# Kernel optimization log

Measured on AMD Instinct MI355X. Metric: run time of the kernel, lower is better.

## Reference

```python
import jax, jax.numpy as jnp
import numpy as np

N, T, E, B = 50000, 16, 800000, 2000
EMB, ENC, DEC, OUT_LEN = 32, 64, 128, 25
NEG_SLOPE = 0.1
BN_EPS = 1e-5


def lrelu(x):
    return jnp.where(x >= 0, x, NEG_SLOPE * x)


def gru_encode(xs, Wih, Whh, bih, bhh):
    # xs: [T, N, in] -> final hidden [N, H]   (torch GRU gate order: r, z, n)
    H = Whh.shape[1]

    def step(h, x_t):
        gi = x_t @ Wih.T + bih
        gh = h @ Whh.T + bhh
        i_r, i_z, i_n = jnp.split(gi, 3, axis=-1)
        h_r, h_z, h_n = jnp.split(gh, 3, axis=-1)
        r = jax.nn.sigmoid(i_r + h_r)
        z = jax.nn.sigmoid(i_z + h_z)
        n = jnp.tanh(i_n + r * h_n)
        return (1.0 - z) * n + z * h, None

    h0 = jnp.zeros((xs.shape[1], H), xs.dtype)
    hT, _ = jax.lax.scan(step, h0, xs)
    return hT


def lstm_layer(xs, Wih, Whh, bih, bhh):
    # xs: [T, B, in] -> outputs [T, B, H]   (torch LSTM gate order: i, f, g, o)
    H = Whh.shape[1]

    def step(carry, x_t):
        h, c = carry
        g = x_t @ Wih.T + bih + h @ Whh.T + bhh
        i, f, gg, o = jnp.split(g, 4, axis=-1)
        c = jax.nn.sigmoid(f) * c + jax.nn.sigmoid(i) * jnp.tanh(gg)
        h = jax.nn.sigmoid(o) * jnp.tanh(c)
        return (h, c), h

    z0 = jnp.zeros((xs.shape[1], H), xs.dtype)
    _, hs = jax.lax.scan(step, (z0, z0), xs)
    return hs


def cgconv(x, src, dst, edge_attr, Wf, bf, Ws, bs, gamma, beta, mean, var):
    # PyG CGConv: z = [x_i, x_j, e]; msg = sigmoid(lin_f(z)) * softplus(lin_s(z));
    # out = x + BN(scatter_add(msg, i))
    z = jnp.concatenate([x[dst], x[src], edge_attr], axis=-1)  # [E, 2*ENC+2]
    msg = jax.nn.sigmoid(z @ Wf.T + bf) * jax.nn.softplus(z @ Ws.T + bs)
    agg = jax.ops.segment_sum(msg, dst, num_segments=N)  # [N, ENC]
    agg = (agg - mean) * jax.lax.rsqrt(var + BN_EPS) * gamma + beta
    return x + agg


def setup_inputs() -> dict:
    key = jax.random.key(0)
    ks = jax.random.split(key, 32)

    def rn(k, shape, scale=0.1):
        return jax.random.normal(k, shape, jnp.float32) * scale

    inp = {}
    inp["x"] = jax.random.normal(ks[0], (N, T, 2), jnp.float32)
    inp["edge_index"] = jax.random.randint(ks[1], (2, E), 0, N)
    inp["edge_attr"] = jax.random.normal(ks[2], (E, 2), jnp.float32)
    inp["target_index"] = jnp.sort(jax.random.randint(ks[3], (B,), 0, N))
    inp["W_ip"] = rn(ks[4], (EMB, 2)); inp["b_ip"] = jnp.zeros((EMB,), jnp.float32)
    inp["gru_Wih"] = rn(ks[5], (3 * ENC, EMB)); inp["gru_Whh"] = rn(ks[6], (3 * ENC, ENC))
    inp["gru_bih"] = jnp.zeros((3 * ENC,), jnp.float32); inp["gru_bhh"] = jnp.zeros((3 * ENC,), jnp.float32)
    inp["W_dyn"] = rn(ks[7], (ENC, ENC)); inp["b_dyn"] = jnp.zeros((ENC,), jnp.float32)
    Z = 2 * ENC + 2
    for i, base in ((1, 8), (2, 14)):
        inp[f"cg{i}_Wf"] = rn(ks[base], (ENC, Z)); inp[f"cg{i}_bf"] = jnp.zeros((ENC,), jnp.float32)
        inp[f"cg{i}_Ws"] = rn(ks[base + 1], (ENC, Z)); inp[f"cg{i}_bs"] = jnp.zeros((ENC,), jnp.float32)
        inp[f"cg{i}_gamma"] = jnp.ones((ENC,), jnp.float32); inp[f"cg{i}_beta"] = jnp.zeros((ENC,), jnp.float32)
        inp[f"cg{i}_mean"] = jnp.zeros((ENC,), jnp.float32); inp[f"cg{i}_var"] = jnp.ones((ENC,), jnp.float32)
    inp["W_nbrs"] = rn(ks[20], (ENC, ENC)); inp["b_nbrs"] = jnp.zeros((ENC,), jnp.float32)
    inp["lstm0_Wih"] = rn(ks[21], (4 * DEC, 2 * ENC)); inp["lstm0_Whh"] = rn(ks[22], (4 * DEC, DEC))
    inp["lstm0_bih"] = jnp.zeros((4 * DEC,), jnp.float32); inp["lstm0_bhh"] = jnp.zeros((4 * DEC,), jnp.float32)
    inp["lstm1_Wih"] = rn(ks[23], (4 * DEC, DEC)); inp["lstm1_Whh"] = rn(ks[24], (4 * DEC, DEC))
    inp["lstm1_bih"] = jnp.zeros((4 * DEC,), jnp.float32); inp["lstm1_bhh"] = jnp.zeros((4 * DEC,), jnp.float32)
    inp["W_op"] = rn(ks[25], (2, DEC)); inp["b_op"] = jnp.zeros((2,), jnp.float32)
    return inp


def reference(x, edge_index, edge_attr, target_index, W_ip, b_ip,
              gru_Wih, gru_Whh, gru_bih, gru_bhh, W_dyn, b_dyn,
              cg1_Wf, cg1_bf, cg1_Ws, cg1_bs, cg1_gamma, cg1_beta, cg1_mean, cg1_var,
              cg2_Wf, cg2_bf, cg2_Ws, cg2_bs, cg2_gamma, cg2_beta, cg2_mean, cg2_var,
              W_nbrs, b_nbrs,
              lstm0_Wih, lstm0_Whh, lstm0_bih, lstm0_bhh,
              lstm1_Wih, lstm1_Whh, lstm1_bih, lstm1_bhh, W_op, b_op):
    src, dst = edge_index[0], edge_index[1]
    # --- history encoder (GRU) ---
    h = lrelu(x @ W_ip.T + b_ip)                                  # [N, T, EMB]
    hT = gru_encode(h.transpose(1, 0, 2), gru_Wih, gru_Whh, gru_bih, gru_bhh)  # [N, ENC]
    hist = lrelu(lrelu(hT) @ W_dyn.T + b_dyn)                     # [N, ENC]
    # --- CGConv interaction x2 ---
    f = cgconv(hist, src, dst, edge_attr, cg1_Wf, cg1_bf, cg1_Ws, cg1_bs,
               cg1_gamma, cg1_beta, cg1_mean, cg1_var)
    f = cgconv(f, src, dst, edge_attr, cg2_Wf, cg2_bf, cg2_Ws, cg2_bs,
               cg2_gamma, cg2_beta, cg2_mean, cg2_var)
    tar = lrelu(f[target_index] @ W_nbrs.T + b_nbrs)              # [B, ENC]
    enc = jnp.concatenate([hist[target_index], tar], axis=-1)     # [B, 2*ENC]
    # --- LSTM decoder over repeated encoding ---
    xs = jnp.broadcast_to(enc, (OUT_LEN,) + enc.shape)            # [OUT_LEN, B, 2*ENC]
    hs = lstm_layer(xs, lstm0_Wih, lstm0_Whh, lstm0_bih, lstm0_bhh)
    hs = lstm_layer(hs, lstm1_Wih, lstm1_Whh, lstm1_bih, lstm1_bhh)
    fut = hs.transpose(1, 0, 2) @ W_op.T + b_op                   # [B, OUT_LEN, 2]
    return fut
```

## Files before the change

kernel.cpp:

```cpp
#include <hip/hip_runtime.h>
#include <math.h>

#define NN   50000
#define TT   16
#define EE   800000
#define BB   2000
#define EMBD 32
#define ENC  64
#define DEC  128
#define OUTL 25
#define BN_EPS 1e-5f

typedef short v8s __attribute__((ext_vector_type(8)));
typedef float v4f __attribute__((ext_vector_type(4)));
#define MFMA16(a,b,c) __builtin_amdgcn_mfma_f32_16x16x32_bf16((a),(b),(c),0,0,0)

__device__ __forceinline__ float lrelu(float v){ return v >= 0.f ? v : 0.1f*v; }
__device__ __forceinline__ float fsig(float v){ return __builtin_amdgcn_rcpf(1.f + __expf(-v)); }
__device__ __forceinline__ float ftanh(float v){ return 2.f*__builtin_amdgcn_rcpf(1.f + __expf(-2.f*v)) - 1.f; }
__device__ __forceinline__ float fsoftplus(float v){
    return v > 15.f ? v : __logf(1.f + __expf(v));
}
__device__ __forceinline__ float hsum(float4 a){ return (a.x+a.y)+(a.z+a.w); }

__device__ __forceinline__ unsigned short f2bf(float f){
    unsigned u = __float_as_uint(f);
    u = u + 0x7FFFu + ((u>>16)&1u);
    return (unsigned short)(u>>16);
}
__device__ __forceinline__ float bf2f(unsigned short s){ return __uint_as_float(((unsigned)s)<<16); }

__device__ __forceinline__ v8s as_v8s(int4 v){
    union { int4 i; v8s s; } u; u.i = v; return u.s;
}

__device__ __forceinline__ void cvt8(const float* p, v8s& hi, v8s& lo){
    float4 a0 = *(const float4*)p;
    float4 a1 = *(const float4*)(p+4);
    float av[8] = {a0.x,a0.y,a0.z,a0.w,a1.x,a1.y,a1.z,a1.w};
#pragma unroll
    for (int j=0;j<8;j++){
        unsigned short h = f2bf(av[j]);
        hi[j] = (short)h;
        lo[j] = (short)f2bf(av[j] - bf2f(h));
    }
}
__device__ __forceinline__ void lrelu_resplit(v8s hh, v8s hl, v8s& oh, v8s& ol){
#pragma unroll
    for (int j=0;j<8;j++){
        float v = bf2f((unsigned short)hh[j]) + bf2f((unsigned short)hl[j]);
        float a = lrelu(v);
        unsigned short h = f2bf(a);
        oh[j] = (short)h;
        ol[j] = (short)f2bf(a - bf2f(h));
    }
}

__device__ __forceinline__ void pf_item(const float* W, int K, int KB, int i,
                                        unsigned short* out){
    int l = i & 63, fb = i >> 6;
    int kb = fb % KB, nt = fb / KB;
    int n = nt*16 + (l&15);
    int k0 = kb*32 + ((l>>4)*8);
#pragma unroll
    for (int j=0;j<8;j++) out[i*8+j] = f2bf(W[(size_t)n*K + k0 + j]);
}
__device__ __forceinline__ void phl_item(const float* W, int K, int KB, int i,
                                         unsigned short* hi, unsigned short* lo){
    int l = i & 63, fb = i >> 6;
    int kb = fb % KB, nt = fb / KB;
    int n = nt*16 + (l&15);
    int k0 = kb*32 + ((l>>4)*8);
#pragma unroll
    for (int j=0;j<8;j++){
        float v = W[(size_t)n*K + k0 + j];
        unsigned short h = f2bf(v);
        hi[i*8+j] = h;
        lo[i*8+j] = f2bf(v - bf2f(h));
    }
}
__device__ __forceinline__ void pcat_item(const float* Wa, const float* Wb,
                                          int K1, int K, int KB, int i,
                                          unsigned short* out){
    int l = i & 63, fb = i >> 6;
    int kb = fb % KB, nt = fb / KB;
    int n = nt*16 + (l&15);
    int k0 = kb*32 + ((l>>4)*8);
#pragma unroll
    for (int j=0;j<8;j++){
        int k = k0 + j;
        float v = (k < K1) ? Wa[(size_t)n*K1 + k] : Wb[(size_t)n*(K-K1) + (k-K1)];
        out[i*8+j] = f2bf(v);
    }
}
__device__ __forceinline__ void pproj_item(const float* Wf, const float* Ws, int i,
                                           unsigned short* hi, unsigned short* lo){
    int l = i & 63, fb = i >> 6;
    int kb = fb & 1, nt = fb >> 1;
    int n = nt*16 + (l&15);
    int d = n >> 6, c = n & 63;
    const float* W = (d < 2) ? Wf : Ws;
    int k0 = (d&1)*64 + kb*32 + ((l>>4)*8);
#pragma unroll
    for (int j=0;j<8;j++){
        float v = W[c*130 + k0 + j];
        unsigned short h = f2bf(v);
        hi[i*8+j] = h;
        lo[i*8+j] = f2bf(v - bf2f(h));
    }
}

__global__ void pack_all(
    const float* __restrict__ gWih, const float* __restrict__ gWhh,
    const float* __restrict__ Wdyn,
    const float* __restrict__ l0Whh, const float* __restrict__ l1Wih,
    const float* __restrict__ l1Whh, const float* __restrict__ l0Wih,
    const float* __restrict__ c1Wf, const float* __restrict__ c1Ws,
    const float* __restrict__ c2Wf, const float* __restrict__ c2Ws,
    unsigned short* __restrict__ pWih, unsigned short* __restrict__ pWhh,
    unsigned short* __restrict__ pWdyn,
    unsigned short* __restrict__ B0h, unsigned short* __restrict__ B1h,
    unsigned short* __restrict__ P1h, unsigned short* __restrict__ P1l,
    unsigned short* __restrict__ P2h, unsigned short* __restrict__ P2l,
    unsigned short* __restrict__ GIh, unsigned short* __restrict__ GIl,
    int* __restrict__ cnt, int* __restrict__ gtot)
{
    int i = blockIdx.x*256 + threadIdx.x;
    if (i < 768){ pf_item(gWih, 32, 1, i, pWih); return; }   i -= 768;
    if (i < 1536){ pf_item(gWhh, 64, 2, i, pWhh); return; }  i -= 1536;
    if (i < 512){ pf_item(Wdyn, 64, 2, i, pWdyn); return; }  i -= 512;
    if (i < 8192){ pcat_item(l0Whh, l0Whh, 128, 128, 4, i, B0h); return; } i -= 8192;
    if (i < 16384){ pcat_item(l1Wih, l1Whh, 128, 256, 8, i, B1h); return; } i -= 16384;
    if (i < 2048){ pproj_item(c1Wf, c1Ws, i, P1h, P1l); return; } i -= 2048;
    if (i < 2048){ pproj_item(c2Wf, c2Ws, i, P2h, P2l); return; } i -= 2048;
    if (i < 8192){ phl_item(l0Wih, 128, 4, i, GIh, GIl); return; } i -= 8192;
    if (i < NN){ cnt[i] = 0; return; } i -= NN;
    if (i < 1){ gtot[0] = 0; return; }
}
#define PACK_TOTAL (768+1536+512+8192+16384+2048+2048+8192+NN+1)

__global__ __launch_bounds__(128) void encoder_mfma(
    const float* __restrict__ x,
    const float* __restrict__ Wip, const float* __restrict__ bip,
    const unsigned short* __restrict__ pWih,
    const unsigned short* __restrict__ pWhh,
    const float* __restrict__ bih, const float* __restrict__ bhh,
    const unsigned short* __restrict__ pWdyn,
    const float* __restrict__ bdyn,
    float* __restrict__ hist)
{
    __shared__ float sxl[512];
    __shared__ unsigned short efh[512], efl[512];
    __shared__ unsigned short hfh[2*512], hfl[2*512];
    const int tid = threadIdx.x;
    const int l   = tid & 63;
    const int w   = tid >> 6;
    const int ln  = l & 15, q = l >> 4;
    const int blk = blockIdx.x;

    ((float4*)sxl)[tid] = ((const float4*)x)[(size_t)blk*128 + tid];
    for (int i=tid;i<2*512;i+=128){ hfh[i]=0; hfl[i]=0; }

    const int ek = tid & 31;
    const float w0 = Wip[2*ek], w1 = Wip[2*ek+1], bk = bip[ek];
    const int em0 = tid >> 5;
    const int eoffb = (16*(ek>>3))*8 + (ek&7);

    float bR[2], bZ[2], bNI[2], bNH[2];
    float hprev[2][4];
#pragma unroll
    for (int u=0;u<2;u++){
        int g = 2*w + u;
        int c = g*16 + ln;
        bR[u]  = bih[c]       + bhh[c];
        bZ[u]  = bih[64 + c]  + bhh[64 + c];
        bNI[u] = bih[128 + c];
        bNH[u] = bhh[128 + c];
        hprev[u][0]=0.f; hprev[u][1]=0.f; hprev[u][2]=0.f; hprev[u][3]=0.f;
    }
    const v8s* FIH = (const v8s*)pWih;
    const v8s* FHH = (const v8s*)pWhh;
    const v8s* FDY = (const v8s*)pWdyn;
    __syncthreads();

#pragma unroll 1
    for (int t=0;t<TT;t++){
#pragma unroll
        for (int r=0;r<4;r++){
            int m = em0 + r*4;
            float e = lrelu(w0*sxl[m*32 + 2*t] + w1*sxl[m*32 + 2*t + 1] + bk);
            unsigned short h_ = f2bf(e);
            int off = eoffb + m*8;
            efh[off] = h_;
            efl[off] = f2bf(e - bf2f(h_));
        }
        __syncthreads();
        v8s eh = *(const v8s*)&efh[l*8];
        v8s el = *(const v8s*)&efl[l*8];
        v8s h0h = *(const v8s*)&hfh[l*8];
        v8s h0l = *(const v8s*)&hfl[l*8];
        v8s h1h = *(const v8s*)&hfh[512 + l*8];
        v8s h1l = *(const v8s*)&hfl[512 + l*8];
        __syncthreads();
#pragma unroll
        for (int u=0;u<2;u++){
            int g = 2*w + u;
            v4f aR = {bR[u],bR[u],bR[u],bR[u]};
            v4f aZ = {bZ[u],bZ[u],bZ[u],bZ[u]};
            v4f aNI= {bNI[u],bNI[u],bNI[u],bNI[u]};
            v4f aNH= {bNH[u],bNH[u],bNH[u],bNH[u]};
            v8s b;
            b = FIH[(g   )*64 + l];   aR = MFMA16(eh,b,aR);  aR = MFMA16(el,b,aR);
            b = FHH[((g)*2+0)*64+l];  aR = MFMA16(h0h,b,aR); aR = MFMA16(h0l,b,aR);
            b = FHH[((g)*2+1)*64+l];  aR = MFMA16(h1h,b,aR); aR = MFMA16(h1l,b,aR);
            b = FIH[(4+g )*64 + l];   aZ = MFMA16(eh,b,aZ);  aZ = MFMA16(el,b,aZ);
            b = FHH[((4+g)*2+0)*64+l];aZ = MFMA16(h0h,b,aZ); aZ = MFMA16(h0l,b,aZ);
            b = FHH[((4+g)*2+1)*64+l];aZ = MFMA16(h1h,b,aZ); aZ = MFMA16(h1l,b,aZ);
            b = FIH[(8+g )*64 + l];   aNI= MFMA16(eh,b,aNI); aNI= MFMA16(el,b,aNI);
            b = FHH[((8+g)*2+0)*64+l];aNH= MFMA16(h0h,b,aNH);aNH= MFMA16(h0l,b,aNH);
            b = FHH[((8+g)*2+1)*64+l];aNH= MFMA16(h1h,b,aNH);aNH= MFMA16(h1l,b,aNH);
#pragma unroll
            for (int i=0;i<4;i++){
                float r_ = fsig(aR[i]);
                float z_ = fsig(aZ[i]);
                float nn_ = ftanh(aNI[i] + r_*aNH[i]);
                float hn = (1.f - z_)*nn_ + z_*hprev[u][i];
                hprev[u][i] = hn;
                int row = q*4 + i, col = g*16 + ln;
                int off = (col>>5)*512 + (16*((col&31)>>3) + row)*8 + (col&7);
                unsigned short hh_ = f2bf(hn);
                hfh[off] = hh_;
                hfl[off] = f2bf(hn - bf2f(hh_));
            }
        }
    }
    __syncthreads();
    {
        v8s a0h,a0l,a1h,a1l;
        lrelu_resplit(*(const v8s*)&hfh[l*8],       *(const v8s*)&hfl[l*8],       a0h, a0l);
        lrelu_resplit(*(const v8s*)&hfh[512 + l*8], *(const v8s*)&hfl[512 + l*8], a1h, a1l);
#pragma unroll
        for (int u=0;u<2;u++){
            int nt = 2*w + u;
            float bb = bdyn[nt*16 + ln];
            v4f acc = {bb,bb,bb,bb};
            v8s b;
            b = FDY[(nt*2+0)*64 + l]; acc = MFMA16(a0h,b,acc); acc = MFMA16(a0l,b,acc);
            b = FDY[(nt*2+1)*64 + l]; acc = MFMA16(a1h,b,acc); acc = MFMA16(a1l,b,acc);
#pragma unroll
            for (int i=0;i<4;i++){
                hist[(size_t)(blk*16 + q*4 + i)*64 + nt*16 + ln] = lrelu(acc[i]);
            }
        }
    }
}

__global__ __launch_bounds__(256) void proj_mfma(
    const float* __restrict__ xin,
    const unsigned short* __restrict__ Bh, const unsigned short* __restrict__ Bl,
    float* __restrict__ Af, float* __restrict__ Bf,
    float* __restrict__ As, float* __restrict__ Bs)
{
    __shared__ float sx[64*68];
    const int tid = threadIdx.x;
    const int l = tid & 63;
    const int w = tid >> 6;
    const int ln = l & 15, q = l >> 4;
    const int n0 = blockIdx.x*64;

    for (int i=tid;i<64*16;i+=256){
        int nn = i>>4, f4 = i&15;
        float4 v = {0.f,0.f,0.f,0.f};
        if (n0+nn < NN) v = ((const float4*)(xin + (size_t)(n0+nn)*64))[f4];
        *(float4*)&sx[nn*68 + f4*4] = v;
    }
    __syncthreads();

    v8s ah0,al0,ah1,al1;
    cvt8(&sx[(w*16+ln)*68 +      q*8], ah0, al0);
    cvt8(&sx[(w*16+ln)*68 + 32 + q*8], ah1, al1);

    const v8s* FH = (const v8s*)Bh;
    const v8s* FL = (const v8s*)Bl;
#pragma unroll 1
    for (int nt=0; nt<16; nt++){
        v8s bh0 = FH[(nt*2+0)*64 + l], bl0 = FL[(nt*2+0)*64 + l];
        v8s bh1 = FH[(nt*2+1)*64 + l], bl1 = FL[(nt*2+1)*64 + l];
        v4f acc = {0.f,0.f,0.f,0.f};
        acc = MFMA16(ah0,bh0,acc); acc = MFMA16(al0,bh0,acc); acc = MFMA16(ah0,bl0,acc);
        acc = MFMA16(ah1,bh1,acc); acc = MFMA16(al1,bh1,acc); acc = MFMA16(ah1,bl1,acc);
        int d = nt >> 2, col = (nt&3)*16 + ln;
        float* op = (d==0) ? Af : (d==1) ? Bf : (d==2) ? As : Bs;
#pragma unroll
        for (int i=0;i<4;i++){
            int node = n0 + w*16 + q*4 + i;
            if (node < NN) op[(size_t)node*64 + col] = acc[i];
        }
    }
}

__global__ void count_kernel(const int* __restrict__ ei, int* __restrict__ cnt){
    int e = blockIdx.x*256 + threadIdx.x;
    if (e < EE) atomicAdd(&cnt[ei[EE+e]], 1);
}

__global__ void alloc_kernel(const int* __restrict__ cnt, int* __restrict__ gtot,
                             int* __restrict__ off, int* __restrict__ cur){
    int n = blockIdx.x*256 + threadIdx.x;
    if (n >= NN) return;
    int c = cnt[n];
    int s = atomicAdd(gtot, c);
    off[n] = s;
    cur[n] = s;
}

__global__ void scatter_kernel(const int* __restrict__ ei, const float* __restrict__ ea,
                               int* __restrict__ cur, int4* __restrict__ recS){
    int e = blockIdx.x*256 + threadIdx.x;
    if (e >= EE) return;
    int d = ei[EE+e];
    int p = atomicAdd(&cur[d], 1);
    int4 r;
    r.x = ei[e];
    r.y = __float_as_int(ea[2*(size_t)e]);
    r.z = __float_as_int(ea[2*(size_t)e+1]);
    r.w = 0;
    recS[p] = r;
}

__global__ __launch_bounds__(256) void cg_agg(
    const float* __restrict__ xin,
    const int4* __restrict__ recS,
    const int* __restrict__ off, const int* __restrict__ cnt,
    const float* __restrict__ Wf, const float* __restrict__ bf,
    const float* __restrict__ Ws, const float* __restrict__ bs,
    const float* __restrict__ Af, const float* __restrict__ Bf,
    const float* __restrict__ As, const float* __restrict__ Bs,
    const float* __restrict__ gamma, const float* __restrict__ beta,
    const float* __restrict__ mean, const float* __restrict__ var,
    float* __restrict__ outp)
{
    const int tid = threadIdx.x;
    const int c = tid & 63, wid = tid >> 6;
    const int n = blockIdx.x*4 + wid;
    if (n >= NN) return;

    const float wf0 = Wf[c*130+128], wf1 = Wf[c*130+129], bfc = bf[c];
    const float ws0 = Ws[c*130+128], ws1 = Ws[c*130+129], bsc = bs[c];
    const float afd = Af[(size_t)n*64+c] + bfc, asd = As[(size_t)n*64+c] + bsc;
    const float* Bfc = Bf + c;
    const float* Bsc = Bs + c;

    float acc = 0.f;
    int i = off[n];
    const int i1 = i + cnt[n];
#pragma unroll 1
    for (; i+1 < i1; i += 2){
        int4 r0 = recS[i], r1 = recS[i+1];
        float e00 = __int_as_float(r0.y), e01 = __int_as_float(r0.z);
        float e10 = __int_as_float(r1.y), e11 = __int_as_float(r1.z);
        float bf0v = Bfc[(size_t)r0.x*64], bs0v = Bsc[(size_t)r0.x*64];
        float bf1v = Bfc[(size_t)r1.x*64], bs1v = Bsc[(size_t)r1.x*64];
        float gf0 = afd + bf0v + wf0*e00 + wf1*e01;
        float gs0 = asd + bs0v + ws0*e00 + ws1*e01;
        float gf1 = afd + bf1v + wf0*e10 + wf1*e11;
        float gs1 = asd + bs1v + ws0*e10 + ws1*e11;
        acc += fsig(gf0)*fsoftplus(gs0);
        acc += fsig(gf1)*fsoftplus(gs1);
    }
    if (i < i1){
        int4 r0 = recS[i];
        float e00 = __int_as_float(r0.y), e01 = __int_as_float(r0.z);
        float gf = afd + Bfc[(size_t)r0.x*64] + wf0*e00 + wf1*e01;
        float gs = asd + Bsc[(size_t)r0.x*64] + ws0*e00 + ws1*e01;
        acc += fsig(gf)*fsoftplus(gs);
    }
    float bn = (acc - mean[c])*rsqrtf(var[c]+BN_EPS)*gamma[c] + beta[c];
    outp[(size_t)n*64+c] = xin[(size_t)n*64+c] + bn;
}

__global__ __launch_bounds__(256) void target_kernel(
    const float* __restrict__ hist, const float* __restrict__ f2,
    const int* __restrict__ tgt,
    const float* __restrict__ Wn, const float* __restrict__ bn_,
    float* __restrict__ enc)
{
    const int tid=threadIdx.x;
    const int c = tid&63, q = tid>>6;
    const int b = blockIdx.x*4 + q;
    if (b>=BB) return;
    const int n = tgt[b];
    float a = bn_[c];
#pragma unroll
    for (int k=0;k<ENC;k++) a += Wn[c*64+k]*f2[(size_t)n*64+k];
    enc[(size_t)b*128 + 64 + c] = lrelu(a);
    enc[(size_t)b*128 + c]      = hist[(size_t)n*64+c];
}

__global__ __launch_bounds__(512) void gi0_mfma(
    const float* __restrict__ enc,
    const unsigned short* __restrict__ GIh, const unsigned short* __restrict__ GIl,
    const float* __restrict__ bih0, const float* __restrict__ bhh0,
    float* __restrict__ gi0)
{
    __shared__ float senc[16*132];
    const int tid = threadIdx.x;
    const int l = tid & 63;
    const int w = tid >> 6;
    const int ln = l & 15, q = l >> 4;
    const int b0 = blockIdx.x*16;

    for (int i=tid;i<16*32;i+=512){
        int row = i>>5, f4 = i&31;
        *(float4*)&senc[row*132 + f4*4] = ((const float4*)(enc + (size_t)(b0+row)*128))[f4];
    }
    __syncthreads();

    v8s ah[4], al[4];
#pragma unroll
    for (int kb=0;kb<4;kb++) cvt8(&senc[ln*132 + kb*32 + q*8], ah[kb], al[kb]);

    const v8s* FH = (const v8s*)GIh;
    const v8s* FL = (const v8s*)GIl;
#pragma unroll
    for (int u=0;u<4;u++){
        int nt = w*4 + u;
        int col = nt*16 + ln;
        float bb = bih0[col] + bhh0[col];
        v4f acc = {bb,bb,bb,bb};
#pragma unroll
        for (int kb=0;kb<4;kb++){
            v8s bh = FH[(nt*4+kb)*64 + l];
            v8s bl = FL[(nt*4+kb)*64 + l];
            acc = MFMA16(ah[kb],bh,acc); acc = MFMA16(al[kb],bh,acc); acc = MFMA16(ah[kb],bl,acc);
        }
#pragma unroll
        for (int i=0;i<4;i++)
            gi0[(size_t)(b0 + q*4 + i)*512 + col] = acc[i];
    }
}

#define LMB 16
__global__ __launch_bounds__(512)
__attribute__((amdgpu_waves_per_eu(2,2)))
void lstm_mfma(
    const float* __restrict__ gi0,
    const unsigned short* __restrict__ B0h,
    const unsigned short* __restrict__ B1h,
    const float* __restrict__ bih1, const float* __restrict__ bhh1,
    const float* __restrict__ Wop, const float* __restrict__ bop,
    float* __restrict__ outp)
{
    __shared__ int4 sW0[32*4*64];
    __shared__ unsigned short h0hi[2][4*512], h0lo[2][4*512];
    __shared__ unsigned short h1hi[2][4*512], h1lo[2][4*512];
    const int tid = threadIdx.x;
    const int l = tid & 63;
    const int w = tid >> 6;
    const int c = l & 15;
    const int q = l >> 4;
    const int j = w*16 + c;
    const int b0 = blockIdx.x*LMB;

    {
        const int4* F0 = (const int4*)B0h;
        for (int i=tid;i<32*4*64;i+=512) sW0[i] = F0[i];
    }
    for (int i=tid;i<4*512;i+=512){
        h0hi[0][i]=0; h0lo[0][i]=0; h0hi[1][i]=0; h0lo[1][i]=0;
        h1hi[0][i]=0; h1lo[0][i]=0; h1hi[1][i]=0; h1lo[1][i]=0;
    }

    int4 W1r[32];
    {
        const int4* F1 = (const int4*)B1h;
#pragma unroll
        for (int g=0;g<4;g++)
#pragma unroll
            for (int kb=0;kb<8;kb++) W1r[g*8+kb] = F1[((g*8+w)*8 + kb)*64 + l];
#pragma unroll
        for (int i=0;i<32;i++)
            asm volatile("" : "+v"(W1r[i].x), "+v"(W1r[i].y), "+v"(W1r[i].z), "+v"(W1r[i].w));
    }

    float rgi[4][4];
#pragma unroll
    for (int g=0;g<4;g++)
#pragma unroll
        for (int i=0;i<4;i++)
            rgi[g][i] = gi0[(size_t)(b0 + q*4 + i)*512 + g*128 + j];

    float b1[4];
#pragma unroll
    for (int g=0;g<4;g++) b1[g] = bih1[g*128+j] + bhh1[g*128+j];
    float c0[4] = {0,0,0,0}, c1[4] = {0,0,0,0};
    const float wop0 = Wop[j], wop1 = Wop[128 + j];
    const float bo0 = bop[0], bo1 = bop[1];
    const int kbw = j>>5, qw = (j>>3)&3, jw = j&7;
    __syncthreads();

    int p = 0;
#pragma unroll 1
    for (int t=0;t<OUTL;t++){
        v4f aH[4], aL[4];
#pragma unroll
        for (int g=0;g<4;g++){
            v4f t4 = {rgi[g][0], rgi[g][1], rgi[g][2], rgi[g][3]};
            aH[g] = t4;
            v4f z = {0.f,0.f,0.f,0.f};
            aL[g] = z;
        }
#pragma unroll
        for (int kb=0;kb<4;kb++){
            v8s ah = *(const v8s*)&h0hi[p][kb*512 + l*8];
            v8s al = *(const v8s*)&h0lo[p][kb*512 + l*8];
#pragma unroll
            for (int g=0;g<4;g++){
                v8s bfr = as_v8s(sW0[((g*8+w)*4 + kb)*64 + l]);
                aH[g] = MFMA16(ah, bfr, aH[g]);
                aL[g] = MFMA16(al, bfr, aL[g]);
            }
        }
#pragma unroll
        for (int i=0;i<4;i++){
            float gi_ = aH[0][i]+aL[0][i], gf_ = aH[1][i]+aL[1][i];
            float gg_ = aH[2][i]+aL[2][i], go_ = aH[3][i]+aL[3][i];
            c0[i] = fsig(gf_)*c0[i] + fsig(gi_)*ftanh(gg_);
            float hn = fsig(go_)*ftanh(c0[i]);
            int off = kbw*512 + (qw*16 + q*4 + i)*8 + jw;
            unsigned short h = f2bf(hn);
            h0hi[1-p][off] = h;
            h0lo[1-p][off] = f2bf(hn - bf2f(h));
        }
        __syncthreads();

        v4f bH[4], bL[4];
#pragma unroll
        for (int g=0;g<4;g++){
            v4f t4={b1[g],b1[g],b1[g],b1[g]}; bH[g]=t4;
            v4f z={0.f,0.f,0.f,0.f}; bL[g]=z;
        }
#pragma unroll
        for (int kb=0;kb<8;kb++){
            const unsigned short* hb = (kb<4) ? h0hi[1-p] : h1hi[p];
            const unsigned short* lb = (kb<4) ? h0lo[1-p] : h1lo[p];
            int kk = kb & 3;
            v8s ah = *(const v8s*)&hb[kk*512 + l*8];
            v8s al = *(const v8s*)&lb[kk*512 + l*8];
#pragma unroll
            for (int g=0;g<4;g++){
                bH[g] = MFMA16(ah, as_v8s(W1r[g*8+kb]), bH[g]);
                bL[g] = MFMA16(al, as_v8s(W1r[g*8+kb]), bL[g]);
            }
        }
        float h1new[4];
#pragma unroll
        for (int i=0;i<4;i++){
            float gi_ = bH[0][i]+bL[0][i], gf_ = bH[1][i]+bL[1][i];
            float gg_ = bH[2][i]+bL[2][i], go_ = bH[3][i]+bL[3][i];
            c1[i] = fsig(gf_)*c1[i] + fsig(gi_)*ftanh(gg_);
            h1new[i] = fsig(go_)*ftanh(c1[i]);
            int off = kbw*512 + (qw*16 + q*4 + i)*8 + jw;
            unsigned short h = f2bf(h1new[i]);
            h1hi[1-p][off] = h;
            h1lo[1-p][off] = f2bf(h1new[i] - bf2f(h));
        }

        {
            float v0[4], v1[4];
#pragma unroll
            for (int i=0;i<4;i++){ v0[i] = h1new[i]*wop0; v1[i] = h1new[i]*wop1; }
#pragma unroll
            for (int m=1;m<16;m<<=1){
#pragma unroll
                for (int i=0;i<4;i++){
                    v0[i] += __shfl_xor(v0[i], m);
                    v1[i] += __shfl_xor(v1[i], m);
                }
            }
            if (c == 0){
                if (w == 0){
#pragma unroll
                    for (int i=0;i<4;i++){ v0[i] += bo0; v1[i] += bo1; }
                }
#pragma unroll
                for (int i=0;i<4;i++){
                    size_t base = (size_t)(b0 + q*4 + i)*(OUTL*2) + t*2;
                    atomicAdd(&outp[base    ], v0[i]);
                    atomicAdd(&outp[base + 1], v1[i]);
                }
            }
        }
        p ^= 1;
    }
}

extern "C" void kernel_launch(void* const* d_in, const int* in_sizes, int n_in,
                              void* d_out, int out_size, void* d_ws, size_t ws_size,
                              hipStream_t stream)
{
    const float* x    = (const float*)d_in[0];
    const int*   ei   = (const int*)d_in[1];
    const float* ea   = (const float*)d_in[2];
    const int*   tgt  = (const int*)d_in[3];
    const float* Wip  = (const float*)d_in[4];
    const float* bip  = (const float*)d_in[5];
    const float* gWih = (const float*)d_in[6];
    const float* gWhh = (const float*)d_in[7];
    const float* gbih = (const float*)d_in[8];
    const float* gbhh = (const float*)d_in[9];
    const float* Wdyn = (const float*)d_in[10];
    const float* bdyn = (const float*)d_in[11];
    const float* c1Wf=(const float*)d_in[12]; const float* c1bf=(const float*)d_in[13];
    const float* c1Ws=(const float*)d_in[14]; const float* c1bs=(const float*)d_in[15];
    const float* c1g =(const float*)d_in[16]; const float* c1b =(const float*)d_in[17];
    const float* c1m =(const float*)d_in[18]; const float* c1v =(const float*)d_in[19];
    const float* c2Wf=(const float*)d_in[20]; const float* c2bf=(const float*)d_in[21];
    const float* c2Ws=(const float*)d_in[22]; const float* c2bs=(const float*)d_in[23];
    const float* c2g =(const float*)d_in[24]; const float* c2b =(const float*)d_in[25];
    const float* c2m =(const float*)d_in[26]; const float* c2v =(const float*)d_in[27];
    const float* Wn  =(const float*)d_in[28]; const float* bn_ =(const float*)d_in[29];
    const float* l0Wih=(const float*)d_in[30]; const float* l0Whh=(const float*)d_in[31];
    const float* l0bih=(const float*)d_in[32]; const float* l0bhh=(const float*)d_in[33];
    const float* l1Wih=(const float*)d_in[34]; const float* l1Whh=(const float*)d_in[35];
    const float* l1bih=(const float*)d_in[36]; const float* l1bhh=(const float*)d_in[37];
    const float* Wop =(const float*)d_in[38]; const float* bop=(const float*)d_in[39];

    float* ws = (float*)d_ws;
    size_t o = 0;
    float* hist = ws + o; o += (size_t)NN*ENC;
    float* f1   = ws + o; o += (size_t)NN*ENC;
    float* f2   = ws + o; o += (size_t)NN*ENC;
    float* Af   = ws + o; o += (size_t)NN*ENC;
    float* Bf   = ws + o; o += (size_t)NN*ENC;
    float* As   = ws + o; o += (size_t)NN*ENC;
    float* Bs   = ws + o; o += (size_t)NN*ENC;
    float* enc  = ws + o; o += (size_t)BB*2*ENC;
    float* gi0  = ws + o; o += (size_t)BB*4*DEC;
    unsigned short* pWih  = (unsigned short*)(ws + o); o += (size_t)12*64*8/2;
    unsigned short* pWhh  = (unsigned short*)(ws + o); o += (size_t)24*64*8/2;
    unsigned short* pWdyn = (unsigned short*)(ws + o); o += (size_t)8*64*8/2;
    unsigned short* B0h = (unsigned short*)(ws + o); o += (size_t)32*4*64*8/2;
    unsigned short* B1h = (unsigned short*)(ws + o); o += (size_t)32*8*64*8/2;
    unsigned short* P1h = (unsigned short*)(ws + o); o += (size_t)2048*8/2;
    unsigned short* P1l = (unsigned short*)(ws + o); o += (size_t)2048*8/2;
    unsigned short* P2h = (unsigned short*)(ws + o); o += (size_t)2048*8/2;
    unsigned short* P2l = (unsigned short*)(ws + o); o += (size_t)2048*8/2;
    unsigned short* GIh = (unsigned short*)(ws + o); o += (size_t)8192*8/2;
    unsigned short* GIl = (unsigned short*)(ws + o); o += (size_t)8192*8/2;
    int* cnt    = (int*)(ws + o); o += NN;
    int* offv   = (int*)(ws + o); o += NN+1;
    int* curv   = (int*)(ws + o); o += NN;
    int* gtot   = (int*)(ws + o); o += 1;
    o = (o + 3) & ~(size_t)3;
    int4* recS  = (int4*)(ws + o); o += (size_t)4*EE;

    pack_all<<<(PACK_TOTAL+255)/256, 256, 0, stream>>>(
        gWih, gWhh, Wdyn, l0Whh, l1Wih, l1Whh, l0Wih,
        c1Wf, c1Ws, c2Wf, c2Ws,
        pWih, pWhh, pWdyn, B0h, B1h, P1h, P1l, P2h, P2l, GIh, GIl, cnt, gtot);

    (void)hipMemsetAsync(d_out, 0, (size_t)out_size*sizeof(float), stream);

    count_kernel<<<(EE+255)/256, 256, 0, stream>>>(ei, cnt);
    alloc_kernel<<<(NN+255)/256, 256, 0, stream>>>(cnt, gtot, offv, curv);
    scatter_kernel<<<(EE+255)/256, 256, 0, stream>>>(ei, ea, curv, recS);

    encoder_mfma<<<NN/16, 128, 0, stream>>>(x, Wip, bip, pWih, pWhh, gbih, gbhh, pWdyn, bdyn, hist);

    proj_mfma<<<(NN+63)/64, 256, 0, stream>>>(hist, P1h, P1l, Af,Bf,As,Bs);
    cg_agg<<<(NN+3)/4, 256, 0, stream>>>(hist, recS, offv, cnt,
                                         c1Wf,c1bf,c1Ws,c1bs, Af,Bf,As,Bs,
                                         c1g,c1b,c1m,c1v, f1);

    proj_mfma<<<(NN+63)/64, 256, 0, stream>>>(f1, P2h, P2l, Af,Bf,As,Bs);
    cg_agg<<<(NN+3)/4, 256, 0, stream>>>(f1, recS, offv, cnt,
                                         c2Wf,c2bf,c2Ws,c2bs, Af,Bf,As,Bs,
                                         c2g,c2b,c2m,c2v, f2);

    target_kernel<<<(BB+3)/4, 256, 0, stream>>>(hist, f2, tgt, Wn, bn_, enc);

    gi0_mfma<<<BB/16, 512, 0, stream>>>(enc, GIh, GIl, l0bih, l0bhh, gi0);

    lstm_mfma<<<BB/LMB, 512, 0, stream>>>(gi0, B0h, B1h,
                                          l1bih, l1bhh, Wop, bop, (float*)d_out);
}
```

Measured before the change: 627.7 us.

## Run GRU encoder with one wavefront per block and register-built embeddings

The GRU encoder block shrinks from two wavefronts to one, and that wave now handles all four 16-column gate groups. The input embedding is computed straight into MFMA A-operand registers from a transposed LDS copy of x, which removes the embedding LDS staging and one barrier per timestep. The fp32-to-bf16 hi/lo split switches from round-to-nearest to a cheaper truncation. In exchange, the grid has half as many waves and each wave runs a longer serial MFMA chain per step, and the split's rounding behaviour changes slightly.

```diff
diff --git a/kernel.cpp b/kernel.cpp
--- a/kernel.cpp
+++ b/kernel.cpp
@@ -29,6 +29,13 @@
     return (unsigned short)(u>>16);
 }
 __device__ __forceinline__ float bf2f(unsigned short s){ return __uint_as_float(((unsigned)s)<<16); }
+
+__device__ __forceinline__ void tsplit(float v, unsigned short& hi, unsigned short& lo){
+    unsigned u = __float_as_uint(v);
+    hi = (unsigned short)(u >> 16);
+    float r = v - __uint_as_float(u & 0xFFFF0000u);
+    lo = (unsigned short)(__float_as_uint(r) >> 16);
+}
 
 __device__ __forceinline__ v8s as_v8s(int4 v){
     union { int4 i; v8s s; } u; u.i = v; return u.s;
@@ -139,7 +146,7 @@
 }
 #define PACK_TOTAL (768+1536+512+8192+16384+2048+2048+8192+NN+1)
 
-__global__ __launch_bounds__(128) void encoder_mfma(
+__global__ __launch_bounds__(64) void encoder_mfma(
     const float* __restrict__ x,
     const float* __restrict__ Wip, const float* __restrict__ bip,
     const unsigned short* __restrict__ pWih,
@@ -149,34 +156,36 @@
     const float* __restrict__ bdyn,
     float* __restrict__ hist)
 {
-    __shared__ float sxl[512];
-    __shared__ unsigned short efh[512], efl[512];
-    __shared__ unsigned short hfh[2*512], hfl[2*512];
+    __shared__ float sxt[512];
+    __shared__ unsigned short hfh[1024], hfl[1024];
     const int tid = threadIdx.x;
-    const int l   = tid & 63;
-    const int w   = tid >> 6;
+    const int l   = tid;
     const int ln  = l & 15, q = l >> 4;
     const int blk = blockIdx.x;
 
-    ((float4*)sxl)[tid] = ((const float4*)x)[(size_t)blk*128 + tid];
-    for (int i=tid;i<2*512;i+=128){ hfh[i]=0; hfl[i]=0; }
-
-    const int ek = tid & 31;
-    const float w0 = Wip[2*ek], w1 = Wip[2*ek+1], bk = bip[ek];
-    const int em0 = tid >> 5;
-    const int eoffb = (16*(ek>>3))*8 + (ek&7);
-
-    float bR[2], bZ[2], bNI[2], bNH[2];
-    float hprev[2][4];
-#pragma unroll
-    for (int u=0;u<2;u++){
-        int g = 2*w + u;
+    for (int idx = tid; idx < 512; idx += 64){
+        int m = idx >> 5, r = idx & 31;
+        sxt[(r>>1)*32 + m*2 + (r&1)] = x[(size_t)blk*512 + idx];
+    }
+    for (int i = tid; i < 1024; i += 64){ hfh[i] = 0; hfl[i] = 0; }
+
+    float w0[8], w1[8], bk[8];
+#pragma unroll
+    for (int j = 0; j < 8; j++){
+        int k = q*8 + j;
+        w0[j] = Wip[2*k]; w1[j] = Wip[2*k+1]; bk[j] = bip[k];
+    }
+
+    float bR[4], bZ[4], bNI[4], bNH[4];
+    float hprev[4][4];
+#pragma unroll
+    for (int g = 0; g < 4; g++){
         int c = g*16 + ln;
-        bR[u]  = bih[c]       + bhh[c];
-        bZ[u]  = bih[64 + c]  + bhh[64 + c];
-        bNI[u] = bih[128 + c];
-        bNH[u] = bhh[128 + c];
-        hprev[u][0]=0.f; hprev[u][1]=0.f; hprev[u][2]=0.f; hprev[u][3]=0.f;
+        bR[g]  = bih[c]       + bhh[c];
+        bZ[g]  = bih[64 + c]  + bhh[64 + c];
+        bNI[g] = bih[128 + c];
+        bNH[g] = bhh[128 + c];
+        hprev[g][0]=0.f; hprev[g][1]=0.f; hprev[g][2]=0.f; hprev[g][3]=0.f;
     }
     const v8s* FIH = (const v8s*)pWih;
     const v8s* FHH = (const v8s*)pWhh;
@@ -184,71 +193,66 @@
     __syncthreads();
 
 #pragma unroll 1
-    for (int t=0;t<TT;t++){
-#pragma unroll
-        for (int r=0;r<4;r++){
-            int m = em0 + r*4;
-            float e = lrelu(w0*sxl[m*32 + 2*t] + w1*sxl[m*32 + 2*t + 1] + bk);
-            unsigned short h_ = f2bf(e);
-            int off = eoffb + m*8;
-            efh[off] = h_;
-            efl[off] = f2bf(e - bf2f(h_));
-        }
-        __syncthreads();
-        v8s eh = *(const v8s*)&efh[l*8];
-        v8s el = *(const v8s*)&efl[l*8];
+    for (int t = 0; t < TT; t++){
+        float2 xv = *(const float2*)&sxt[t*32 + ln*2];
+        v8s eh, el;
+#pragma unroll
+        for (int j = 0; j < 8; j++){
+            float e = lrelu(w0[j]*xv.x + w1[j]*xv.y + bk[j]);
+            unsigned short h_, l_;
+            tsplit(e, h_, l_);
+            eh[j] = (short)h_; el[j] = (short)l_;
+        }
         v8s h0h = *(const v8s*)&hfh[l*8];
         v8s h0l = *(const v8s*)&hfl[l*8];
         v8s h1h = *(const v8s*)&hfh[512 + l*8];
         v8s h1l = *(const v8s*)&hfl[512 + l*8];
-        __syncthreads();
-#pragma unroll
-        for (int u=0;u<2;u++){
-            int g = 2*w + u;
-            v4f aR = {bR[u],bR[u],bR[u],bR[u]};
-            v4f aZ = {bZ[u],bZ[u],bZ[u],bZ[u]};
-            v4f aNI= {bNI[u],bNI[u],bNI[u],bNI[u]};
-            v4f aNH= {bNH[u],bNH[u],bNH[u],bNH[u]};
+#pragma unroll
+        for (int g = 0; g < 4; g++){
+            v4f aR = {bR[g],bR[g],bR[g],bR[g]};
+            v4f aZ = {bZ[g],bZ[g],bZ[g],bZ[g]};
+            v4f aNI= {bNI[g],bNI[g],bNI[g],bNI[g]};
+            v4f aNH= {bNH[g],bNH[g],bNH[g],bNH[g]};
             v8s b;
-            b = FIH[(g   )*64 + l];   aR = MFMA16(eh,b,aR);  aR = MFMA16(el,b,aR);
-            b = FHH[((g)*2+0)*64+l];  aR = MFMA16(h0h,b,aR); aR = MFMA16(h0l,b,aR);
-            b = FHH[((g)*2+1)*64+l];  aR = MFMA16(h1h,b,aR); aR = MFMA16(h1l,b,aR);
-            b = FIH[(4+g )*64 + l];   aZ = MFMA16(eh,b,aZ);  aZ = MFMA16(el,b,aZ);
-            b = FHH[((4+g)*2+0)*64+l];aZ = MFMA16(h0h,b,aZ); aZ = MFMA16(h0l,b,aZ);
-            b = FHH[((4+g)*2+1)*64+l];aZ = MFMA16(h1h,b,aZ); aZ = MFMA16(h1l,b,aZ);
-            b = FIH[(8+g )*64 + l];   aNI= MFMA16(eh,b,aNI); aNI= MFMA16(el,b,aNI);
-            b = FHH[((8+g)*2+0)*64+l];aNH= MFMA16(h0h,b,aNH);aNH= MFMA16(h0l,b,aNH);
-            b = FHH[((8+g)*2+1)*64+l];aNH= MFMA16(h1h,b,aNH);aNH= MFMA16(h1l,b,aNH);
-#pragma unroll
-            for (int i=0;i<4;i++){
+            b = FIH[(g   )*64 + l];    aR = MFMA16(eh,b,aR);  aR = MFMA16(el,b,aR);
+            b = FHH[(g*2+0)*64+l];     aR = MFMA16(h0h,b,aR); aR = MFMA16(h0l,b,aR);
+            b = FHH[(g*2+1)*64+l];     aR = MFMA16(h1h,b,aR); aR = MFMA16(h1l,b,aR);
+            b = FIH[(4+g )*64 + l];    aZ = MFMA16(eh,b,aZ);  aZ = MFMA16(el,b,aZ);
+            b = FHH[((4+g)*2+0)*64+l]; aZ = MFMA16(h0h,b,aZ); aZ = MFMA16(h0l,b,aZ);
+            b = FHH[((4+g)*2+1)*64+l]; aZ = MFMA16(h1h,b,aZ); aZ = MFMA16(h1l,b,aZ);
+            b = FIH[(8+g )*64 + l];    aNI= MFMA16(eh,b,aNI); aNI= MFMA16(el,b,aNI);
+            b = FHH[((8+g)*2+0)*64+l]; aNH= MFMA16(h0h,b,aNH);aNH= MFMA16(h0l,b,aNH);
+            b = FHH[((8+g)*2+1)*64+l]; aNH= MFMA16(h1h,b,aNH);aNH= MFMA16(h1l,b,aNH);
+#pragma unroll
+            for (int i = 0; i < 4; i++){
                 float r_ = fsig(aR[i]);
                 float z_ = fsig(aZ[i]);
                 float nn_ = ftanh(aNI[i] + r_*aNH[i]);
-                float hn = (1.f - z_)*nn_ + z_*hprev[u][i];
-                hprev[u][i] = hn;
+                float hn = (1.f - z_)*nn_ + z_*hprev[g][i];
+                hprev[g][i] = hn;
                 int row = q*4 + i, col = g*16 + ln;
                 int off = (col>>5)*512 + (16*((col&31)>>3) + row)*8 + (col&7);
-                unsigned short hh_ = f2bf(hn);
+                unsigned short hh_, hl_;
+                tsplit(hn, hh_, hl_);
                 hfh[off] = hh_;
-                hfl[off] = f2bf(hn - bf2f(hh_));
+                hfl[off] = hl_;
             }
         }
-    }
-    __syncthreads();
+        __syncthreads();
+    }
     {
         v8s a0h,a0l,a1h,a1l;
         lrelu_resplit(*(const v8s*)&hfh[l*8],       *(const v8s*)&hfl[l*8],       a0h, a0l);
         lrelu_resplit(*(const v8s*)&hfh[512 + l*8], *(const v8s*)&hfl[512 + l*8], a1h, a1l);
 #pragma unroll
-        for (int u=0;u<2;u++){
-            int nt = 2*w + u;
+        for (int nt = 0; nt < 4; nt++){
             float bb = bdyn[nt*16 + ln];
             v4f acc = {bb,bb,bb,bb};
             v8s b;
             b = FDY[(nt*2+0)*64 + l]; acc = MFMA16(a0h,b,acc); acc = MFMA16(a0l,b,acc);
             b = FDY[(nt*2+1)*64 + l]; acc = MFMA16(a1h,b,acc); acc = MFMA16(a1l,b,acc);
 #pragma unroll
-            for (int i=0;i<4;i++){
+            for (int i = 0; i < 4; i++){
                 hist[(size_t)(blk*16 + q*4 + i)*64 + nt*16 + ln] = lrelu(acc[i]);
             }
         }
@@ -666,7 +670,7 @@
     alloc_kernel<<<(NN+255)/256, 256, 0, stream>>>(cnt, gtot, offv, curv);
     scatter_kernel<<<(EE+255)/256, 256, 0, stream>>>(ei, ea, curv, recS);
 
-    encoder_mfma<<<NN/16, 128, 0, stream>>>(x, Wip, bip, pWih, pWhh, gbih, gbhh, pWdyn, bdyn, hist);
+    encoder_mfma<<<NN/16, 64, 0, stream>>>(x, Wip, bip, pWih, pWhh, gbih, gbhh, pWdyn, bdyn, hist);
 
     proj_mfma<<<(NN+63)/64, 256, 0, stream>>>(hist, P1h, P1l, Af,Bf,As,Bs);
     cg_agg<<<(NN+3)/4, 256, 0, stream>>>(hist, recS, offv, cnt,
```

Result: slower. 640.4 us (+2.0%).
